# Kernel tuning notes

Hardware: AMD Instinct MI355X
Metric: run time of the kernel (lower is better)

The kernel has to match this reference:

```python
import jax, jax.numpy as jnp
import numpy as np

N_NODES = 100000


def setup_inputs() -> dict:
    key = jax.random.key(0)
    k1, k2, k3, k4, k5 = jax.random.split(key, 5)
    embeds = jax.random.normal(k1, (N_NODES, 128), dtype=jnp.float32)
    W = jax.random.normal(k2, (128, 128), dtype=jnp.float32) * (1.0 / np.sqrt(128.0))
    adj_rows = jax.random.randint(k3, (1600000,), 0, N_NODES, dtype=jnp.int32)
    adj_cols = jax.random.randint(k4, (1600000,), 0, N_NODES, dtype=jnp.int32)
    adj_vals = jax.random.uniform(k5, (1600000,), dtype=jnp.float32)
    return {"embeds": embeds, "W": W, "adj_rows": adj_rows,
            "adj_cols": adj_cols, "adj_vals": adj_vals}


def reference(embeds, W, adj_rows, adj_cols, adj_vals):
    # Linear (no bias): h = embeds @ W^T   [N, d]
    h = jnp.einsum('nd,od->no', embeds, W)
    # SpMM: out[r] = sum_{e: rows[e]==r} vals[e] * h[cols[e]]
    msgs = adj_vals[:, None] * h[adj_cols]          # [E, d] gather
    agg = jax.ops.segment_sum(msgs, adj_rows, num_segments=N_NODES)
    # fused leaky_relu, negative_slope=0.2
    return jnp.where(agg >= 0, agg, 0.2 * agg)
```

## Files before the change

### kernel.cpp

```cpp
#include <hip/hip_runtime.h>
#include <hip/hip_bf16.h>

#define D 128
#define PROWS 64
#define CAP 2048
#define NPART_MAX 2048
#define PASSA_EPT 24

typedef __attribute__((ext_vector_type(8))) short short8;
typedef __attribute__((ext_vector_type(4))) float f32x4;

__device__ __forceinline__ short f2bf(float f) {
  __hip_bfloat16 h = __float2bfloat16(f);
  return (short)*reinterpret_cast<unsigned short*>(&h);
}
__device__ __forceinline__ float bf2f(unsigned short u) {
  union { unsigned i; float f; } x;
  x.i = ((unsigned)u) << 16;
  return x.f;
}

__global__ __launch_bounds__(256) void gemm_mfma_bf16_kernel(
    const float* __restrict__ emb, const float* __restrict__ W,
    unsigned short* __restrict__ H2, int N) {
  __shared__ short8 WldsV[2048];
  char* Wlds = (char*)WldsV;
  const int tid = threadIdx.x;

  for (int i = tid; i < 128 * 16; i += 256) {
    int o = i >> 4, dblk = i & 15;
    const float* wp = W + o * D + dblk * 8;
    float4 f0 = *(const float4*)wp;
    float4 f1 = *(const float4*)(wp + 4);
    short8 u;
    u[0] = f2bf(f0.x); u[1] = f2bf(f0.y); u[2] = f2bf(f0.z); u[3] = f2bf(f0.w);
    u[4] = f2bf(f1.x); u[5] = f2bf(f1.y); u[6] = f2bf(f1.z); u[7] = f2bf(f1.w);
    *(short8*)(Wlds + o * 256 + ((dblk ^ (o & 7)) << 4)) = u;
  }
  __syncthreads();

  const int w = tid >> 6, l = tid & 63;
  const int lo = l & 15, hi = l >> 4;
  const int mbase = blockIdx.x * 64 + w * 16;

  int arow = mbase + lo;
  if (arow >= N) arow = N - 1;
  const float* ap = emb + (size_t)arow * D + hi * 8;

  float4 a0[4], a1[4];
#pragma unroll
  for (int kb = 0; kb < 4; ++kb) {
    a0[kb] = *(const float4*)(ap + kb * 32);
    a1[kb] = *(const float4*)(ap + kb * 32 + 4);
  }

  f32x4 acc[8];
#pragma unroll
  for (int ot = 0; ot < 8; ++ot) acc[ot] = (f32x4){0.f, 0.f, 0.f, 0.f};

  const char* brow = Wlds + lo * 256;
#pragma unroll
  for (int kb = 0; kb < 4; ++kb) {
    short8 a;
    a[0] = f2bf(a0[kb].x); a[1] = f2bf(a0[kb].y);
    a[2] = f2bf(a0[kb].z); a[3] = f2bf(a0[kb].w);
    a[4] = f2bf(a1[kb].x); a[5] = f2bf(a1[kb].y);
    a[6] = f2bf(a1[kb].z); a[7] = f2bf(a1[kb].w);
    const int xb = (((kb << 2) | hi) ^ (l & 7)) << 4;
#pragma unroll
    for (int ot = 0; ot < 8; ++ot) {
      short8 b = *(const short8*)(brow + ot * 4096 + xb);
      acc[ot] = __builtin_amdgcn_mfma_f32_16x16x32_bf16(a, b, acc[ot], 0, 0, 0);
    }
  }

  const int rowout = mbase + hi * 4;
#pragma unroll
  for (int r = 0; r < 4; ++r) {
    int ro = rowout + r;
    if (ro < N) {
      unsigned short* op = H2 + (size_t)ro * D + lo;
#pragma unroll
      for (int ot = 0; ot < 8; ++ot) op[ot * 16] = (unsigned short)f2bf(acc[ot][r]);
    }
  }
}

__global__ __launch_bounds__(256) void init_cursor_kernel(int* __restrict__ cursor,
                                                          int npart) {
  int i = blockIdx.x * 256 + threadIdx.x;
  if (i < npart) cursor[i] = i * CAP;
}

__global__ __launch_bounds__(256) void part_scatter_direct_kernel(
    const int* __restrict__ rows, const int* __restrict__ cols,
    const float* __restrict__ vals, int* __restrict__ cursor,
    float2* __restrict__ slots, int E, int npart) {
  __shared__ int cnt[NPART_MAX];
  __shared__ int bas[NPART_MAX];
  for (int i = threadIdx.x; i < npart; i += 256) cnt[i] = 0;
  __syncthreads();
  int base = blockIdx.x * (256 * PASSA_EPT);
#pragma unroll
  for (int k = 0; k < PASSA_EPT; ++k) {
    int idx = base + k * 256 + threadIdx.x;
    if (idx < E) atomicAdd(&cnt[rows[idx] >> 6], 1);
  }
  __syncthreads();
  for (int i = threadIdx.x; i < npart; i += 256) {
    int c = cnt[i];
    bas[i] = c ? atomicAdd(&cursor[i], c) : 0;
    cnt[i] = 0;
  }
  __syncthreads();
#pragma unroll
  for (int k = 0; k < PASSA_EPT; ++k) {
    int idx = base + k * 256 + threadIdx.x;
    if (idx < E) {
      int r = rows[idx];
      int p = r >> 6;
      int rank = atomicAdd(&cnt[p], 1);
      int pos = bas[p] + rank;
      if (pos < (p + 1) * CAP) {
        float2 m;
        m.x = __int_as_float(cols[idx] | ((r & 63) << 17));
        m.y = vals[idx];
        slots[pos] = m;
      }
    }
  }
}

__global__ __launch_bounds__(256) void spmm_part_kernel(
    const unsigned short* __restrict__ H2, const int* __restrict__ cursor,
    const float2* __restrict__ slots, float* __restrict__ out, int N) {
  __shared__ float2 sorted[CAP];
  __shared__ int cnt[PROWS];
  __shared__ int rowofs[PROWS];
  __shared__ int cnt2[PROWS];

  int p = blockIdx.x;
  int t = threadIdx.x;
  const float2* slice = slots + (size_t)p * CAP;
  int ne = cursor[p] - p * CAP;
  if (ne > CAP) ne = CAP;

  if (t < PROWS) { cnt[t] = 0; cnt2[t] = 0; }
  __syncthreads();

  for (int j = t; j < ne; j += 256) {
    int rl = (__float_as_int(slice[j].x) >> 17) & 63;
    atomicAdd(&cnt[rl], 1);
  }
  __syncthreads();

  if (t < 64) {
    int v = cnt[t];
    int x = v;
#pragma unroll
    for (int dd = 1; dd < 64; dd <<= 1) {
      int y = __shfl_up(x, dd, 64);
      if (t >= dd) x += y;
    }
    rowofs[t] = x - v;
  }
  __syncthreads();

  for (int j = t; j < ne; j += 256) {
    float2 m = slice[j];
    int rl = (__float_as_int(m.x) >> 17) & 63;
    int rank = atomicAdd(&cnt2[rl], 1);
    sorted[rowofs[rl] + rank] = m;
  }
  __syncthreads();

  int w = t >> 6, l = t & 63;
  for (int rr = 0; rr < 16; ++rr) {
    int rl = w * 16 + rr;
    int row = p * PROWS + rl;
    if (row >= N) break;
    int s = rowofs[rl];
    int e = s + cnt[rl];
    float ax = 0.f, ay = 0.f;
    int j = s;
    for (; j + 4 <= e; j += 4) {
      float2 m0 = sorted[j];
      float2 m1 = sorted[j + 1];
      float2 m2 = sorted[j + 2];
      float2 m3 = sorted[j + 3];
      int c0 = __float_as_int(m0.x) & 0x1FFFF;
      int c1 = __float_as_int(m1.x) & 0x1FFFF;
      int c2 = __float_as_int(m2.x) & 0x1FFFF;
      int c3 = __float_as_int(m3.x) & 0x1FFFF;
      ushort2 x0 = *(const ushort2*)(H2 + (size_t)c0 * D + 2 * l);
      ushort2 x1 = *(const ushort2*)(H2 + (size_t)c1 * D + 2 * l);
      ushort2 x2 = *(const ushort2*)(H2 + (size_t)c2 * D + 2 * l);
      ushort2 x3 = *(const ushort2*)(H2 + (size_t)c3 * D + 2 * l);
      ax = fmaf(m0.y, bf2f(x0.x), ax); ay = fmaf(m0.y, bf2f(x0.y), ay);
      ax = fmaf(m1.y, bf2f(x1.x), ax); ay = fmaf(m1.y, bf2f(x1.y), ay);
      ax = fmaf(m2.y, bf2f(x2.x), ax); ay = fmaf(m2.y, bf2f(x2.y), ay);
      ax = fmaf(m3.y, bf2f(x3.x), ax); ay = fmaf(m3.y, bf2f(x3.y), ay);
    }
    for (; j < e; ++j) {
      float2 m = sorted[j];
      int c = __float_as_int(m.x) & 0x1FFFF;
      ushort2 x = *(const ushort2*)(H2 + (size_t)c * D + 2 * l);
      ax = fmaf(m.y, bf2f(x.x), ax); ay = fmaf(m.y, bf2f(x.y), ay);
    }
    ax = ax >= 0.f ? ax : 0.2f * ax;
    ay = ay >= 0.f ? ay : 0.2f * ay;
    float2 o;
    o.x = ax;
    o.y = ay;
    ((float2*)(out + (size_t)row * D))[l] = o;
  }
}

__global__ __launch_bounds__(256) void gemm_mfma_f32_kernel(
    const float* __restrict__ emb, const float* __restrict__ W,
    float* __restrict__ H, int N) {
  __shared__ short8 WldsV[2048];
  char* Wlds = (char*)WldsV;
  const int tid = threadIdx.x;
  for (int i = tid; i < 128 * 16; i += 256) {
    int o = i >> 4, dblk = i & 15;
    const float* wp = W + o * D + dblk * 8;
    float4 f0 = *(const float4*)wp;
    float4 f1 = *(const float4*)(wp + 4);
    short8 u;
    u[0] = f2bf(f0.x); u[1] = f2bf(f0.y); u[2] = f2bf(f0.z); u[3] = f2bf(f0.w);
    u[4] = f2bf(f1.x); u[5] = f2bf(f1.y); u[6] = f2bf(f1.z); u[7] = f2bf(f1.w);
    *(short8*)(Wlds + o * 256 + ((dblk ^ (o & 7)) << 4)) = u;
  }
  __syncthreads();
  const int w = tid >> 6, l = tid & 63;
  const int lo = l & 15, hi = l >> 4;
  const int mbase = blockIdx.x * 64 + w * 16;
  int arow = mbase + lo;
  if (arow >= N) arow = N - 1;
  const float* ap = emb + (size_t)arow * D + hi * 8;
  float4 a0[4], a1[4];
#pragma unroll
  for (int kb = 0; kb < 4; ++kb) {
    a0[kb] = *(const float4*)(ap + kb * 32);
    a1[kb] = *(const float4*)(ap + kb * 32 + 4);
  }
  f32x4 acc[8];
#pragma unroll
  for (int ot = 0; ot < 8; ++ot) acc[ot] = (f32x4){0.f, 0.f, 0.f, 0.f};
  const char* brow = Wlds + lo * 256;
#pragma unroll
  for (int kb = 0; kb < 4; ++kb) {
    short8 a;
    a[0] = f2bf(a0[kb].x); a[1] = f2bf(a0[kb].y);
    a[2] = f2bf(a0[kb].z); a[3] = f2bf(a0[kb].w);
    a[4] = f2bf(a1[kb].x); a[5] = f2bf(a1[kb].y);
    a[6] = f2bf(a1[kb].z); a[7] = f2bf(a1[kb].w);
    const int xb = (((kb << 2) | hi) ^ (l & 7)) << 4;
#pragma unroll
    for (int ot = 0; ot < 8; ++ot) {
      short8 b = *(const short8*)(brow + ot * 4096 + xb);
      acc[ot] = __builtin_amdgcn_mfma_f32_16x16x32_bf16(a, b, acc[ot], 0, 0, 0);
    }
  }
  const int rowout = mbase + hi * 4;
#pragma unroll
  for (int r = 0; r < 4; ++r) {
    int ro = rowout + r;
    if (ro < N) {
      float* op = H + (size_t)ro * D + lo;
#pragma unroll
      for (int ot = 0; ot < 8; ++ot) op[ot * 16] = acc[ot][r];
    }
  }
}

__global__ __launch_bounds__(256) void spmm_scatter_kernel(
    const float* __restrict__ H, const int* __restrict__ rows,
    const int* __restrict__ cols, const float* __restrict__ vals,
    float* __restrict__ out, int E) {
  long long gid = (long long)blockIdx.x * blockDim.x + threadIdx.x;
  int e = (int)(gid >> 5);
  int l = (int)(gid & 31);
  if (e >= E) return;
  int r = rows[e];
  int c = cols[e];
  float v = vals[e];
  float4 h4 = ((const float4*)(H + (size_t)c * D))[l];
  float* op = out + (size_t)r * D + l * 4;
  atomicAdd(op + 0, v * h4.x);
  atomicAdd(op + 1, v * h4.y);
  atomicAdd(op + 2, v * h4.z);
  atomicAdd(op + 3, v * h4.w);
}

__global__ __launch_bounds__(256) void leaky_kernel(float* __restrict__ out,
                                                    int n4) {
  for (int i = blockIdx.x * blockDim.x + threadIdx.x; i < n4;
       i += gridDim.x * blockDim.x) {
    float4 v = ((const float4*)out)[i];
    v.x = v.x >= 0.f ? v.x : 0.2f * v.x;
    v.y = v.y >= 0.f ? v.y : 0.2f * v.y;
    v.z = v.z >= 0.f ? v.z : 0.2f * v.z;
    v.w = v.w >= 0.f ? v.w : 0.2f * v.w;
    ((float4*)out)[i] = v;
  }
}

extern "C" void kernel_launch(void* const* d_in, const int* in_sizes, int n_in,
                              void* d_out, int out_size, void* d_ws,
                              size_t ws_size, hipStream_t stream) {
  const float* emb  = (const float*)d_in[0];
  const float* W    = (const float*)d_in[1];
  const int*   rows = (const int*)d_in[2];
  const int*   cols = (const int*)d_in[3];
  const float* vals = (const float*)d_in[4];
  float* out = (float*)d_out;

  int N = in_sizes[0] / D;
  int E = in_sizes[2];
  int npart = (N + PROWS - 1) / PROWS;

  char* p = (char*)d_ws;
  auto carve = [&](size_t bytes) {
    char* r = p;
    p += (bytes + 255) & ~(size_t)255;
    return r;
  };
  unsigned short* H2     = (unsigned short*)carve((size_t)N * D * 2);
  int*            cursor = (int*)carve((size_t)npart * sizeof(int));
  float2*         slots  = (float2*)carve((size_t)npart * CAP * sizeof(float2));
  size_t needed = (size_t)(p - (char*)d_ws);

  int gblocks = (N + 63) / 64;
  int nb_edge = (E + 256 * PASSA_EPT - 1) / (256 * PASSA_EPT);

  if (needed <= ws_size && npart <= NPART_MAX && N <= (1 << 17)) {
    gemm_mfma_bf16_kernel<<<gblocks, 256, 0, stream>>>(emb, W, H2, N);
    init_cursor_kernel<<<(npart + 255) / 256, 256, 0, stream>>>(cursor, npart);
    part_scatter_direct_kernel<<<nb_edge, 256, 0, stream>>>(rows, cols, vals,
                                                            cursor, slots, E,
                                                            npart);
    spmm_part_kernel<<<npart, 256, 0, stream>>>(H2, cursor, slots, out, N);
  } else {
    float* Hf = (float*)d_ws;
    gemm_mfma_f32_kernel<<<gblocks, 256, 0, stream>>>(emb, W, Hf, N);
    hipMemsetAsync(d_out, 0, (size_t)N * D * sizeof(float), stream);
    long long sthreads = (long long)E * 32;
    int sblocks = (int)((sthreads + 255) / 256);
    spmm_scatter_kernel<<<sblocks, 256, 0, stream>>>(Hf, rows, cols, vals, out, E);
    leaky_kernel<<<1024, 256, 0, stream>>>(out, N * D / 4);
  }
}
```

Before: 126.9 us.

## Fuse GEMM and edge partition scatter into one launch with bf16 W prep

Merges the bf16 GEMM and the edge-bucketing scatter into one kernel whose blocks are split by index between the two jobs, so the two independent phases run side by side. A small prep kernel converts W to bf16 once and zeroes the cursors, so GEMM blocks read bf16 W straight from global or cache instead of staging and converting it in LDS. The SpMM kernel now keeps each thread's slot entries in registers between the counting and sorting passes, removing the second global read. The trade-off is cached global reads of W in place of swizzled LDS loads, and a fused kernel that reserves the scatter's 16 KB of shared memory for GEMM blocks too, which can lower their occupancy.

```diff
diff --git a/kernel.cpp b/kernel.cpp
--- a/kernel.cpp
+++ b/kernel.cpp
@@ -20,112 +20,101 @@
   return x.f;
 }
 
-__global__ __launch_bounds__(256) void gemm_mfma_bf16_kernel(
-    const float* __restrict__ emb, const float* __restrict__ W,
-    unsigned short* __restrict__ H2, int N) {
-  __shared__ short8 WldsV[2048];
-  char* Wlds = (char*)WldsV;
-  const int tid = threadIdx.x;
-
-  for (int i = tid; i < 128 * 16; i += 256) {
-    int o = i >> 4, dblk = i & 15;
-    const float* wp = W + o * D + dblk * 8;
-    float4 f0 = *(const float4*)wp;
-    float4 f1 = *(const float4*)(wp + 4);
-    short8 u;
-    u[0] = f2bf(f0.x); u[1] = f2bf(f0.y); u[2] = f2bf(f0.z); u[3] = f2bf(f0.w);
-    u[4] = f2bf(f1.x); u[5] = f2bf(f1.y); u[6] = f2bf(f1.z); u[7] = f2bf(f1.w);
-    *(short8*)(Wlds + o * 256 + ((dblk ^ (o & 7)) << 4)) = u;
-  }
-  __syncthreads();
-
-  const int w = tid >> 6, l = tid & 63;
-  const int lo = l & 15, hi = l >> 4;
-  const int mbase = blockIdx.x * 64 + w * 16;
-
-  int arow = mbase + lo;
-  if (arow >= N) arow = N - 1;
-  const float* ap = emb + (size_t)arow * D + hi * 8;
-
-  float4 a0[4], a1[4];
-#pragma unroll
-  for (int kb = 0; kb < 4; ++kb) {
-    a0[kb] = *(const float4*)(ap + kb * 32);
-    a1[kb] = *(const float4*)(ap + kb * 32 + 4);
-  }
-
-  f32x4 acc[8];
-#pragma unroll
-  for (int ot = 0; ot < 8; ++ot) acc[ot] = (f32x4){0.f, 0.f, 0.f, 0.f};
-
-  const char* brow = Wlds + lo * 256;
-#pragma unroll
-  for (int kb = 0; kb < 4; ++kb) {
-    short8 a;
-    a[0] = f2bf(a0[kb].x); a[1] = f2bf(a0[kb].y);
-    a[2] = f2bf(a0[kb].z); a[3] = f2bf(a0[kb].w);
-    a[4] = f2bf(a1[kb].x); a[5] = f2bf(a1[kb].y);
-    a[6] = f2bf(a1[kb].z); a[7] = f2bf(a1[kb].w);
-    const int xb = (((kb << 2) | hi) ^ (l & 7)) << 4;
-#pragma unroll
-    for (int ot = 0; ot < 8; ++ot) {
-      short8 b = *(const short8*)(brow + ot * 4096 + xb);
-      acc[ot] = __builtin_amdgcn_mfma_f32_16x16x32_bf16(a, b, acc[ot], 0, 0, 0);
-    }
-  }
-
-  const int rowout = mbase + hi * 4;
-#pragma unroll
-  for (int r = 0; r < 4; ++r) {
-    int ro = rowout + r;
-    if (ro < N) {
-      unsigned short* op = H2 + (size_t)ro * D + lo;
-#pragma unroll
-      for (int ot = 0; ot < 8; ++ot) op[ot * 16] = (unsigned short)f2bf(acc[ot][r]);
-    }
-  }
-}
-
-__global__ __launch_bounds__(256) void init_cursor_kernel(int* __restrict__ cursor,
-                                                          int npart) {
+__global__ __launch_bounds__(256) void prep_kernel(
+    const float* __restrict__ W, unsigned short* __restrict__ W2,
+    int* __restrict__ cursor, int npart) {
   int i = blockIdx.x * 256 + threadIdx.x;
-  if (i < npart) cursor[i] = i * CAP;
-}
-
-__global__ __launch_bounds__(256) void part_scatter_direct_kernel(
-    const int* __restrict__ rows, const int* __restrict__ cols,
-    const float* __restrict__ vals, int* __restrict__ cursor,
-    float2* __restrict__ slots, int E, int npart) {
+  if (i < D * D) W2[i] = (unsigned short)f2bf(W[i]);
+  if (i < npart) cursor[i] = 0;
+}
+
+__global__ __launch_bounds__(256) void fused_gemm_scatter_kernel(
+    const float* __restrict__ emb, const unsigned short* __restrict__ W2,
+    unsigned short* __restrict__ H2, const int* __restrict__ rows,
+    const int* __restrict__ cols, const float* __restrict__ vals,
+    int* __restrict__ cursor, float2* __restrict__ slots,
+    int E, int N, int npart, int nb_edge) {
   __shared__ int cnt[NPART_MAX];
   __shared__ int bas[NPART_MAX];
-  for (int i = threadIdx.x; i < npart; i += 256) cnt[i] = 0;
-  __syncthreads();
-  int base = blockIdx.x * (256 * PASSA_EPT);
-#pragma unroll
-  for (int k = 0; k < PASSA_EPT; ++k) {
-    int idx = base + k * 256 + threadIdx.x;
-    if (idx < E) atomicAdd(&cnt[rows[idx] >> 6], 1);
-  }
-  __syncthreads();
-  for (int i = threadIdx.x; i < npart; i += 256) {
-    int c = cnt[i];
-    bas[i] = c ? atomicAdd(&cursor[i], c) : 0;
-    cnt[i] = 0;
-  }
-  __syncthreads();
-#pragma unroll
-  for (int k = 0; k < PASSA_EPT; ++k) {
-    int idx = base + k * 256 + threadIdx.x;
-    if (idx < E) {
-      int r = rows[idx];
-      int p = r >> 6;
-      int rank = atomicAdd(&cnt[p], 1);
-      int pos = bas[p] + rank;
-      if (pos < (p + 1) * CAP) {
-        float2 m;
-        m.x = __int_as_float(cols[idx] | ((r & 63) << 17));
-        m.y = vals[idx];
-        slots[pos] = m;
+  const int tid = threadIdx.x;
+
+  if ((int)blockIdx.x < nb_edge) {
+    for (int i = tid; i < npart; i += 256) cnt[i] = 0;
+    __syncthreads();
+    int base = blockIdx.x * (256 * PASSA_EPT);
+#pragma unroll
+    for (int k = 0; k < PASSA_EPT; ++k) {
+      int idx = base + k * 256 + tid;
+      if (idx < E) atomicAdd(&cnt[rows[idx] >> 6], 1);
+    }
+    __syncthreads();
+    for (int i = tid; i < npart; i += 256) {
+      int c = cnt[i];
+      bas[i] = c ? atomicAdd(&cursor[i], c) : 0;
+      cnt[i] = 0;
+    }
+    __syncthreads();
+#pragma unroll
+    for (int k = 0; k < PASSA_EPT; ++k) {
+      int idx = base + k * 256 + tid;
+      if (idx < E) {
+        int r = rows[idx];
+        int p = r >> 6;
+        int rank = atomicAdd(&cnt[p], 1);
+        int off = bas[p] + rank;
+        if (off < CAP) {
+          float2 m;
+          m.x = __int_as_float(cols[idx] | ((r & 63) << 17));
+          m.y = vals[idx];
+          slots[(size_t)p * CAP + off] = m;
+        }
+      }
+    }
+  } else {
+    int bid = blockIdx.x - nb_edge;
+    const int w = tid >> 6, l = tid & 63;
+    const int lo = l & 15, hi = l >> 4;
+    const int mbase = bid * 64 + w * 16;
+
+    int arow = mbase + lo;
+    if (arow >= N) arow = N - 1;
+    const float* ap = emb + (size_t)arow * D + hi * 8;
+
+    float4 a0[4], a1[4];
+#pragma unroll
+    for (int kb = 0; kb < 4; ++kb) {
+      a0[kb] = *(const float4*)(ap + kb * 32);
+      a1[kb] = *(const float4*)(ap + kb * 32 + 4);
+    }
+
+    f32x4 acc[8];
+#pragma unroll
+    for (int ot = 0; ot < 8; ++ot) acc[ot] = (f32x4){0.f, 0.f, 0.f, 0.f};
+
+#pragma unroll
+    for (int kb = 0; kb < 4; ++kb) {
+      short8 a;
+      a[0] = f2bf(a0[kb].x); a[1] = f2bf(a0[kb].y);
+      a[2] = f2bf(a0[kb].z); a[3] = f2bf(a0[kb].w);
+      a[4] = f2bf(a1[kb].x); a[5] = f2bf(a1[kb].y);
+      a[6] = f2bf(a1[kb].z); a[7] = f2bf(a1[kb].w);
+#pragma unroll
+      for (int ot = 0; ot < 8; ++ot) {
+        short8 b = *(const short8*)(W2 + (size_t)(ot * 16 + lo) * D + kb * 32 +
+                                    hi * 8);
+        acc[ot] = __builtin_amdgcn_mfma_f32_16x16x32_bf16(a, b, acc[ot], 0, 0, 0);
+      }
+    }
+
+    const int rowout = mbase + hi * 4;
+#pragma unroll
+    for (int r = 0; r < 4; ++r) {
+      int ro = rowout + r;
+      if (ro < N) {
+        unsigned short* op = H2 + (size_t)ro * D + lo;
+#pragma unroll
+        for (int ot = 0; ot < 8; ++ot)
+          op[ot * 16] = (unsigned short)f2bf(acc[ot][r]);
       }
     }
   }
@@ -142,15 +131,20 @@
   int p = blockIdx.x;
   int t = threadIdx.x;
   const float2* slice = slots + (size_t)p * CAP;
-  int ne = cursor[p] - p * CAP;
+  int ne = cursor[p];
   if (ne > CAP) ne = CAP;
 
   if (t < PROWS) { cnt[t] = 0; cnt2[t] = 0; }
   __syncthreads();
 
-  for (int j = t; j < ne; j += 256) {
-    int rl = (__float_as_int(slice[j].x) >> 17) & 63;
-    atomicAdd(&cnt[rl], 1);
+  float2 my[CAP / 256];
+#pragma unroll
+  for (int k = 0; k < CAP / 256; ++k) {
+    int j = t + k * 256;
+    if (j < ne) {
+      my[k] = slice[j];
+      atomicAdd(&cnt[(__float_as_int(my[k].x) >> 17) & 63], 1);
+    }
   }
   __syncthreads();
 
@@ -166,11 +160,14 @@
   }
   __syncthreads();
 
-  for (int j = t; j < ne; j += 256) {
-    float2 m = slice[j];
-    int rl = (__float_as_int(m.x) >> 17) & 63;
-    int rank = atomicAdd(&cnt2[rl], 1);
-    sorted[rowofs[rl] + rank] = m;
+#pragma unroll
+  for (int k = 0; k < CAP / 256; ++k) {
+    int j = t + k * 256;
+    if (j < ne) {
+      int rl = (__float_as_int(my[k].x) >> 17) & 63;
+      int rank = atomicAdd(&cnt2[rl], 1);
+      sorted[rowofs[rl] + rank] = my[k];
+    }
   }
   __syncthreads();
 
@@ -328,6 +325,7 @@
     return r;
   };
   unsigned short* H2     = (unsigned short*)carve((size_t)N * D * 2);
+  unsigned short* W2     = (unsigned short*)carve((size_t)D * D * 2);
   int*            cursor = (int*)carve((size_t)npart * sizeof(int));
   float2*         slots  = (float2*)carve((size_t)npart * CAP * sizeof(float2));
   size_t needed = (size_t)(p - (char*)d_ws);
@@ -336,11 +334,9 @@
   int nb_edge = (E + 256 * PASSA_EPT - 1) / (256 * PASSA_EPT);
 
   if (needed <= ws_size && npart <= NPART_MAX && N <= (1 << 17)) {
-    gemm_mfma_bf16_kernel<<<gblocks, 256, 0, stream>>>(emb, W, H2, N);
-    init_cursor_kernel<<<(npart + 255) / 256, 256, 0, stream>>>(cursor, npart);
-    part_scatter_direct_kernel<<<nb_edge, 256, 0, stream>>>(rows, cols, vals,
-                                                            cursor, slots, E,
-                                                            npart);
+    prep_kernel<<<(D * D + 255) / 256, 256, 0, stream>>>(W, W2, cursor, npart);
+    fused_gemm_scatter_kernel<<<nb_edge + gblocks, 256, 0, stream>>>(
+        emb, W2, H2, rows, cols, vals, cursor, slots, E, N, npart, nb_edge);
     spmm_part_kernel<<<npart, 256, 0, stream>>>(H2, cursor, slots, out, N);
   } else {
     float* Hf = (float*)d_ws;
```

Result: no change. 129.1 us (+1.8%).
